# Kernel optimization log

Measured on AMD Instinct MI355X. Metric: run time of the kernel, lower is better.

Reference implementation:

```python
import jax, jax.numpy as jnp
import numpy as np
from jax import lax

B, C, H, W = 16, 256, 80, 80
MID = 64
BN_EPS = 1e-5

SOBEL_X = jnp.array([[-1., 0., 1.], [-2., 0., 2.], [-1., 0., 1.]], jnp.float32) / 8.0
SOBEL_Y = jnp.array([[-1., -2., -1.], [0., 0., 0.], [1., 2., 1.]], jnp.float32) / 8.0
HAAR_LH = jnp.array([[1., -1.], [1., -1.]], jnp.float32) / 2.0
HAAR_HL = jnp.array([[1., 1.], [-1., -1.]], jnp.float32) / 2.0

DN = ('NCHW', 'OIHW', 'NCHW')

def dwconv(x, k2d, pad):
    # depthwise conv: same 2d kernel applied to every channel independently
    c = x.shape[1]
    k = jnp.broadcast_to(k2d[None, None], (c, 1) + k2d.shape)
    return lax.conv_general_dilated(x, k, (1, 1), [(pad, pad), (pad, pad)],
                                    dimension_numbers=DN, feature_group_count=c)

def avg_pool5(x):
    # matches F.avg_pool2d(k=5, s=1, p=2) with count_include_pad=True (divide by 25 always)
    s = lax.reduce_window(x, 0.0, lax.add, (1, 1, 5, 5), (1, 1, 1, 1),
                          [(0, 0), (0, 0), (2, 2), (2, 2)])
    return s / 25.0

def local_variance(x):
    m = avg_pool5(x)
    msq = avg_pool5(x * x)
    return jnp.clip(msq - m * m, 0.0, None)

def bn_silu(x, g, b, m, v):
    # inference batchnorm + SiLU, per-channel params over dim 1
    scale = (g / jnp.sqrt(v + BN_EPS))[None, :, None, None]
    shift = (b - m * g / jnp.sqrt(v + BN_EPS))[None, :, None, None]
    return jax.nn.silu(x * scale + shift)

def setup_inputs() -> dict:
    key = jax.random.key(0)
    ks = jax.random.split(key, 12)
    return {
        'x': jax.random.normal(ks[0], (B, C, H, W), jnp.float32),
        'proj_w': jax.random.normal(ks[1], (MID, C), jnp.float32) * 0.05,
        'bn1_g': jax.random.uniform(ks[2], (MID,), jnp.float32),
        'bn1_b': jax.random.normal(ks[3], (MID,), jnp.float32) * 0.1,
        'bn1_m': jax.random.normal(ks[4], (MID,), jnp.float32) * 0.1,
        'bn1_v': jax.random.uniform(ks[5], (MID,), jnp.float32) + 0.5,
        'fuse1_w': jax.random.normal(ks[6], (MID, MID + 2, 3, 3), jnp.float32) * 0.05,
        'bn2_g': jax.random.uniform(ks[7], (MID,), jnp.float32),
        'bn2_b': jax.random.normal(ks[8], (MID,), jnp.float32) * 0.1,
        'bn2_m': jax.random.normal(ks[9], (MID,), jnp.float32) * 0.1,
        'bn2_v': jax.random.uniform(ks[10], (MID,), jnp.float32) + 0.5,
        'fuse2_w': jax.random.normal(ks[11], (1, MID), jnp.float32) * 0.1,
    }

def reference(x, proj_w, bn1_g, bn1_b, bn1_m, bn1_v,
              fuse1_w, bn2_g, bn2_b, bn2_m, bn2_v, fuse2_w):
    b, c, h, w = x.shape
    # --- edge density ---
    gx = dwconv(x, SOBEL_X, 1)
    gy = dwconv(x, SOBEL_Y, 1)
    edge = jnp.sqrt(gx * gx + gy * gy).mean(axis=1, keepdims=True)  # (B,1,H,W)
    edge_density = edge / (avg_pool5(edge) + 1e-6)
    # --- periodicity ---
    lh = dwconv(x, HAAR_LH, 0)  # (B,C,H-1,W-1)
    hl = dwconv(x, HAAR_HL, 0)
    lh = jax.image.resize(lh, (b, c, h, w), method='bilinear')  # half-pixel, matches align_corners=False
    hl = jax.image.resize(hl, (b, c, h, w), method='bilinear')
    period = jnp.sqrt(local_variance(lh) + local_variance(hl) + 1e-6).mean(axis=1, keepdims=True)
    # --- feat_proj: 1x1 conv + BN + SiLU ---
    feat = bn_silu(jnp.einsum('bchw,mc->bmhw', x, proj_w), bn1_g, bn1_b, bn1_m, bn1_v)
    # --- fuse: 3x3 conv + BN + SiLU -> 1x1 conv -> sigmoid ---
    combined = jnp.concatenate([feat, edge_density, period], axis=1)  # (B,MID+2,H,W)
    y = lax.conv_general_dilated(combined, fuse1_w, (1, 1), [(1, 1), (1, 1)], dimension_numbers=DN)
    y = bn_silu(y, bn2_g, bn2_b, bn2_m, bn2_v)
    weight = jax.nn.sigmoid(jnp.einsum('bmhw,om->bohw', y, fuse2_w))  # (B,1,H,W)
    return x * weight
```

## Files before the change

### kernel.cpp

```cpp
#include <hip/hip_runtime.h>
#include <hip/hip_bf16.h>
#include <math.h>

#define HWN 6400
#define CC 256
#define MIDN 64
#define NCG 64

typedef _Float16 f16x8 __attribute__((ext_vector_type(8)));
typedef _Float16 f16x4 __attribute__((ext_vector_type(4)));
typedef _Float16 h2    __attribute__((ext_vector_type(2)));
typedef float    f32x4 __attribute__((ext_vector_type(4)));
typedef int      i32x4 __attribute__((ext_vector_type(4)));

__device__ __forceinline__ h2 pk2(float a, float b) {
    return __builtin_bit_cast(h2, __builtin_amdgcn_cvt_pkrtz(a, b));
}
__device__ __forceinline__ float h2lo(h2 v) { return (float)v[0]; }
__device__ __forceinline__ float h2hi(h2 v) { return (float)v[1]; }
__device__ __forceinline__ unsigned h2u(h2 v) { return __builtin_bit_cast(unsigned, v); }
__device__ __forceinline__ h2 u2h(unsigned u) { return __builtin_bit_cast(h2, u); }
__device__ __forceinline__ float vsqrtf_(float x) { float r; asm("v_sqrt_f32 %0, %1" : "=v"(r) : "v"(x)); return r; }

__global__ void prep_kernel(const float* __restrict__ proj_w,
                            const float* __restrict__ g1, const float* __restrict__ b1,
                            const float* __restrict__ m1, const float* __restrict__ v1,
                            const float* __restrict__ f1w,
                            const float* __restrict__ g2, const float* __restrict__ b2,
                            const float* __restrict__ m2, const float* __restrict__ v2,
                            _Float16* __restrict__ apack_proj,
                            _Float16* __restrict__ apack_fuse,
                            float* __restrict__ bias1, float* __restrict__ bias2) {
    int gid = blockIdx.x * blockDim.x + threadIdx.x;
    int stride = gridDim.x * blockDim.x;
    if (gid < MIDN) {
        float s1 = g1[gid] * rsqrtf(v1[gid] + 1e-5f);
        bias1[gid] = b1[gid] - m1[gid] * s1;
        float s2 = g2[gid] * rsqrtf(v2[gid] + 1e-5f);
        bias2[gid] = b2[gid] - m2[gid] * s2;
    }
    for (int i = gid; i < 8 * 4 * 64 * 8; i += stride) {
        int j = i & 7, lane = (i >> 3) & 63, w = (i >> 9) & 3, c = i >> 11;
        int m = w * 16 + (lane & 15);
        int ch = c * 32 + (lane >> 4) * 8 + j;
        float s1 = g1[m] * rsqrtf(v1[m] + 1e-5f);
        apack_proj[i] = (_Float16)(proj_w[m * CC + ch] * s1);
    }
    for (int i = gid; i < 9 * 3 * 4 * 64 * 8; i += stride) {
        int j = i & 7, lane = (i >> 3) & 63, w = (i >> 9) & 3;
        int tc = i >> 11; int c = tc % 3, t = tc / 3;
        int m = w * 16 + (lane & 15);
        int ch = c * 32 + (lane >> 4) * 8 + j;
        float s2 = g2[m] * rsqrtf(v2[m] + 1e-5f);
        float v = 0.f;
        if (ch < 66) v = f1w[(m * 66 + ch) * 9 + t] * s2;
        apack_fuse[i] = (_Float16)v;
    }
}

__launch_bounds__(512, 4)
__global__ void edge_period_kernel(const float* __restrict__ x,
                                   unsigned* __restrict__ part) {
    __shared__ unsigned wb[8][88];
    volatile unsigned (*wbv)[88] = wb;
    int tid = threadIdx.x;
    int w = tid >> 6, l = tid & 63;
    int b = blockIdx.y, cg = blockIdx.x;
    int row0 = w * 10;
    int im1 = (l + 63) & 63, ip1 = (l + 1) & 63;
    bool is0 = (l == 0), is63 = (l == 63), isB = (l < 16);

    if (l < 4) wbv[w][(l < 2) ? l : 80 + l] = 0u;

    float cwA = (l <= 0) ? 1.f : ((l >= 79) ? 0.f : (0.99375f - 0.0125f * (float)l));
    int cB = 64 + l;
    float cwB = (cB >= 79) ? 0.f : (0.99375f - 0.0125f * (float)cB);
    h2 v_pk = pk2(0.5f * cwA, 0.5f * cwB);
    h2 u_pk = pk2(0.5f * (1.f - cwA), 0.5f * (1.f - cwB));

    h2 erh[10], prh[10];
#pragma unroll
    for (int k = 0; k < 10; k++) { erh[k] = u2h(0u); prh[k] = u2h(0u); }

#pragma unroll 1
    for (int ch = 0; ch < 4; ch++) {
        const float* xch = x + ((size_t)(b * CC + cg * 4 + ch)) * HWN;
        auto rawload = [&](int rr, float& a, float& bb) {
            a = 0.f; bb = 0.f;
            if (rr >= 0 && rr < 80) {
                a = xch[rr * 80 + l];
                if (isB) bb = xch[rr * 80 + 64 + l];
            }
        };
        auto mktrip = [&](float a, float bb, h2& t0, h2& t1, h2& t2) {
            h2 xc = pk2(a, bb);
            int xi = __builtin_bit_cast(int, xc);
            unsigned um = (unsigned)__shfl(xi, im1);
            unsigned up = (unsigned)__shfl(xi, ip1);
            um = is0 ? ((um & 0xFFFFu) << 16) : um;
            up = is63 ? (up >> 16) : up;
            t0 = u2h(um); t1 = xc; t2 = u2h(up);
        };
        h2 xm1_0, xm1_1, xm1_2, x0_0, x0_1, x0_2, xp1_0, xp1_1, xp1_2;
        float ta, tb, ra, rb, na, nb;
        rawload(row0 - 3, ta, tb);
        rawload(row0 - 2, ra, rb);
        mktrip(ta, tb, xm1_0, xm1_1, xm1_2);
        mktrip(ra, rb, x0_0, x0_1, x0_2);
        rawload(row0 - 1, ra, rb);
        h2 lhc_p, hlc_p;
        {
            h2 sa = xm1_0 + x0_0, sb = xm1_1 + x0_1, sc2 = xm1_2 + x0_2;
            h2 da = xm1_0 - x0_0, db = xm1_1 - x0_1, dc = xm1_2 - x0_2;
            lhc_p = u_pk * (sa - sb) + v_pk * (sb - sc2);
            hlc_p = u_pk * (da + db) + v_pk * (db + dc);
        }
        h2 ringA[5], ringB[5], ringS[5];
#pragma unroll
        for (int s = 0; s < 14; s++) {
            int r = row0 - 2 + s;
            if (s < 13) rawload(row0 + s, na, nb);
            mktrip(ra, rb, xp1_0, xp1_1, xp1_2);
            if (s >= 2 && s < 12) {
                h2 gx = (xm1_2 - xm1_0) + (x0_2 - x0_0) + (x0_2 - x0_0) + (xp1_2 - xp1_0);
                h2 gy = (xp1_0 - xm1_0) + (xp1_1 - xm1_1) + (xp1_1 - xm1_1) + (xp1_2 - xm1_2);
                h2 g2v = gx * gx + gy * gy;
                erh[s - 2] += pk2(vsqrtf_(h2lo(g2v)) * 0.125f, vsqrtf_(h2hi(g2v)) * 0.125f);
            }
            h2 sa = x0_0 + xp1_0, sb = x0_1 + xp1_1, sc2 = x0_2 + xp1_2;
            h2 da = x0_0 - xp1_0, db = x0_1 - xp1_1, dc = x0_2 - xp1_2;
            h2 lhc = u_pk * (sa - sb) + v_pk * (sb - sc2);
            h2 hlc = u_pk * (da + db) + v_pk * (db + dc);
            float cw = (r <= 0) ? 1.f : ((r >= 79) ? 0.f : (0.99375f - 0.0125f * (float)r));
            h2 cwp = pk2(cw, cw), pwp = pk2(1.f - cw, 1.f - cw);
            h2 lhr = pwp * lhc_p + cwp * lhc;
            h2 hlr = pwp * hlc_p + cwp * hlc;
            lhc_p = lhc; hlc_p = hlc;
            unsigned lu = h2u(lhr), hu = h2u(hlr);
            unsigned fA = (lu & 0xFFFFu) | (hu << 16);
            unsigned fB = (lu >> 16) | (hu & 0xFFFF0000u);
            bool fv = (r >= 0) && (r < 80);
            if (!fv) { fA = 0u; fB = 0u; }
            wbv[w][2 + l] = fA;
            if (isB) wbv[w][66 + l] = fB;
            unsigned am2 = wbv[w][l], am1 = wbv[w][l + 1], ap1 = wbv[w][l + 3], ap2 = wbv[w][l + 4];
            unsigned bm2 = 0, bm1 = 0, bp1 = 0, bp2 = 0;
            if (isB) { bm2 = wbv[w][64 + l]; bm1 = wbv[w][65 + l]; bp1 = wbv[w][67 + l]; bp2 = wbv[w][68 + l]; }
            h2 fAh = u2h(fA), fBh = u2h(fB);
            h2 n0 = u2h(am2), n1 = u2h(am1), n2 = u2h(ap1), n3 = u2h(ap2);
            h2 hA = fAh + n0 + n1 + n2 + n3;
            h2 qa = fAh * fAh + n0 * n0 + n1 * n1 + n2 * n2 + n3 * n3;
            float s2A = h2lo(qa) + h2hi(qa);
            h2 m0 = u2h(bm2), m1 = u2h(bm1), m2 = u2h(bp1), m3 = u2h(bp2);
            h2 hB = fBh + m0 + m1 + m2 + m3;
            h2 qb = fBh * fBh + m0 * m0 + m1 * m1 + m2 * m2 + m3 * m3;
            float s2B = h2lo(qb) + h2hi(qb);
            ringA[s % 5] = hA; ringB[s % 5] = hB;
            ringS[s % 5] = pk2(s2A, s2B);
            if (s >= 4) {
                h2 SA = ringA[0] + ringA[1] + ringA[2] + ringA[3] + ringA[4];
                h2 SB = ringB[0] + ringB[1] + ringB[2] + ringB[3] + ringB[4];
                h2 S2 = ringS[0] + ringS[1] + ringS[2] + ringS[3] + ringS[4];
                float SLA = h2lo(SA), SHA = h2hi(SA);
                float SLB = h2lo(SB), SHB = h2hi(SB);
                float vA = 0.04f * h2lo(S2) - 0.0016f * (SLA * SLA + SHA * SHA);
                float vB = 0.04f * h2hi(S2) - 0.0016f * (SLB * SLB + SHB * SHB);
                vA = fmaxf(vA, 0.f) + 1e-6f;
                vB = fmaxf(vB, 0.f) + 1e-6f;
                prh[s - 4] += pk2(vsqrtf_(vA), vsqrtf_(vB));
            }
            xm1_0 = x0_0; xm1_1 = x0_1; xm1_2 = x0_2;
            x0_0 = xp1_0; x0_1 = xp1_1; x0_2 = xp1_2;
            ra = na; rb = nb;
        }
    }
    size_t base = ((size_t)(cg * 16 + b) * 80 + row0) * 80;
#pragma unroll
    for (int k = 0; k < 10; k++) {
        unsigned eu = h2u(erh[k]), pu = h2u(prh[k]);
        part[base + k * 80 + l] = (eu & 0xFFFFu) | (pu << 16);
        if (isB) part[base + k * 80 + 64 + l] = (eu >> 16) | (pu & 0xFFFF0000u);
    }
}

__launch_bounds__(256)
__global__ void density_kernel(const unsigned* __restrict__ part,
                               _Float16* __restrict__ feat_t) {
    __shared__ float E[14][84];
    __shared__ float Hs[14][84];
    __shared__ float Ps[10][80];
    int band = blockIdx.x, b = blockIdx.y, tid = threadIdx.x;
    int r0 = band * 10;
    if (tid < 56) { int rr = tid >> 2, c4 = tid & 3; E[rr][(c4 < 2) ? c4 : 80 + c4] = 0.f; }
    for (int idx = tid; idx < 14 * 80; idx += 256) {
        int rr = idx / 80, j = idx - rr * 80;
        int row = r0 - 2 + rr;
        float e = 0.f, p = 0.f;
        if (row >= 0 && row < 80) {
            size_t off = ((size_t)b * 80 + row) * 80 + j;
#pragma unroll 4
            for (int g = 0; g < NCG; g++) {
                h2 v = u2h(part[(size_t)g * (16 * 80 * 80) + off]);
                e += h2lo(v); p += h2hi(v);
            }
        }
        E[rr][2 + j] = e * (1.f / 256.f);
        if (rr >= 2 && rr < 12) Ps[rr - 2][j] = p * (1.f / 256.f);
    }
    __syncthreads();
    for (int idx = tid; idx < 14 * 80; idx += 256) {
        int rr = idx / 80, j = idx - rr * 80;
        Hs[rr][2 + j] = E[rr][j] + E[rr][j + 1] + E[rr][j + 2] + E[rr][j + 3] + E[rr][j + 4];
    }
    __syncthreads();
    for (int idx = tid; idx < 10 * 80; idx += 256) {
        int k = idx / 80, j = idx - k * 80;
        int rr = k + 2;
        float pool = Hs[rr - 2][2 + j] + Hs[rr - 1][2 + j] + Hs[rr][2 + j]
                   + Hs[rr + 1][2 + j] + Hs[rr + 2][2 + j];
        float ed = E[rr][2 + j] / (pool * 0.04f + 1e-6f);
        _Float16* fp = feat_t + ((size_t)(b * HWN) + (r0 + k) * 80 + j) * 96;
        f16x8 z8 = {};
        f16x8 f8 = {};
        f8[0] = (_Float16)ed; f8[1] = (_Float16)Ps[k][j];
        *reinterpret_cast<f16x8*>(fp + 64) = f8;
        *reinterpret_cast<f16x8*>(fp + 72) = z8;
        *reinterpret_cast<f16x8*>(fp + 80) = z8;
        *reinterpret_cast<f16x8*>(fp + 88) = z8;
    }
}

__launch_bounds__(256)
__global__ void proj_kernel(const float* __restrict__ x,
                            const _Float16* __restrict__ apack,
                            const float* __restrict__ bias1,
                            _Float16* __restrict__ feat_t) {
    __shared__ __align__(16) unsigned char lds[64 * 512];
    int b = blockIdx.y, p0 = blockIdx.x * 64;
    int tid = threadIdx.x, w = tid >> 6, l = tid & 63;

#pragma unroll 4
    for (int i = 0; i < 16; i++) {
        int ch0 = i * 16 + w * 4;
        f16x4 v4;
#pragma unroll
        for (int q = 0; q < 4; q++)
            v4[q] = (_Float16)x[((size_t)(b * CC + ch0 + q)) * HWN + p0 + l];
        int byte = l * 512 + ((ch0 * 2) ^ ((l & 7) << 4));
        *reinterpret_cast<f16x4*>(lds + byte) = v4;
    }
    __syncthreads();

    const f16x8* Ap = reinterpret_cast<const f16x8*>(apack);
    f32x4 acc[4];
#pragma unroll
    for (int ct = 0; ct < 4; ct++) acc[ct] = (f32x4){0.f, 0.f, 0.f, 0.f};

    int kb = 16 * (l >> 4);
#pragma unroll 2
    for (int c = 0; c < 8; c++) {
        f16x8 a = Ap[(c * 4 + w) * 64 + l];
#pragma unroll
        for (int ct = 0; ct < 4; ct++) {
            int byte = (ct * 16 + (l & 15)) * 512 + ((c * 64 + kb) ^ ((l & 7) << 4));
            f16x8 bv = *reinterpret_cast<const f16x8*>(lds + byte);
            acc[ct] = __builtin_amdgcn_mfma_f32_16x16x32_f16(a, bv, acc[ct], 0, 0, 0);
        }
    }

    float b1v[4];
#pragma unroll
    for (int q = 0; q < 4; q++) b1v[q] = bias1[w * 16 + (l >> 4) * 4 + q];
#pragma unroll
    for (int ct = 0; ct < 4; ct++) {
        f16x4 o4;
#pragma unroll
        for (int q = 0; q < 4; q++) {
            float z = acc[ct][q] + b1v[q];
            o4[q] = (_Float16)(z / (1.f + expf(-z)));
        }
        size_t px = (size_t)(b * HWN) + p0 + ct * 16 + (l & 15);
        *reinterpret_cast<f16x4*>(feat_t + px * 96 + w * 16 + (l >> 4) * 4) = o4;
    }
}

#define TROW 256
__launch_bounds__(256)
__global__ void fuse_kernel(const _Float16* __restrict__ feat_t,
                            const _Float16* __restrict__ apack,
                            const float* __restrict__ bias2,
                            const float* __restrict__ fuse2,
                            const float* __restrict__ x,
                            float* __restrict__ out) {
    __shared__ __align__(16) unsigned char tl[108 * TROW];
    __shared__ float R[4 * 4 * 4 * 16];
    __shared__ float wgtbuf[64];
    int b = blockIdx.y, t5 = blockIdx.x;
    int ti = t5 / 5, tj = t5 - ti * 5;
    int i0 = ti * 4, j0 = tj * 16;
    int tid = threadIdx.x, w = tid >> 6, l = tid & 63;

    for (int idx = tid; idx < 1296; idx += 256) {
        int hpx = idx / 12, g = idx - hpx * 12;
        int hr = hpx / 18, hc = hpx - hr * 18;
        int gi = i0 - 1 + hr, gj = j0 - 1 + hc;
        i32x4 val = {0, 0, 0, 0};
        if (gi >= 0 && gi < 80 && gj >= 0 && gj < 80) {
            val = *reinterpret_cast<const i32x4*>(
                feat_t + ((size_t)(b * HWN) + gi * 80 + gj) * 96 + g * 8);
        }
        *reinterpret_cast<i32x4*>(tl + hpx * TROW + ((g * 16) ^ ((hc & 7) << 4))) = val;
    }
    __syncthreads();

    const f16x8* Ap = reinterpret_cast<const f16x8*>(apack);
    f32x4 acc[4];
#pragma unroll
    for (int r = 0; r < 4; r++) acc[r] = (f32x4){0.f, 0.f, 0.f, 0.f};
    int kb = 16 * (l >> 4);

#pragma unroll 1
    for (int t = 0; t < 9; t++) {
        int dy = t / 3, dx = t - dy * 3;
        f16x8 a0 = Ap[((t * 3 + 0) * 4 + w) * 64 + l];
        f16x8 a1 = Ap[((t * 3 + 1) * 4 + w) * 64 + l];
        f16x8 a2 = Ap[((t * 3 + 2) * 4 + w) * 64 + l];
        int hc = (l & 15) + dx;
        int key = (hc & 7) << 4;
#pragma unroll
        for (int r = 0; r < 4; r++) {
            int base = ((r + dy) * 18 + hc) * TROW;
            f16x8 b0 = *reinterpret_cast<const f16x8*>(tl + base + ((0 + kb) ^ key));
            acc[r] = __builtin_amdgcn_mfma_f32_16x16x32_f16(a0, b0, acc[r], 0, 0, 0);
            f16x8 b1_ = *reinterpret_cast<const f16x8*>(tl + base + ((64 + kb) ^ key));
            acc[r] = __builtin_amdgcn_mfma_f32_16x16x32_f16(a1, b1_, acc[r], 0, 0, 0);
            f16x8 b2_ = *reinterpret_cast<const f16x8*>(tl + base + ((128 + kb) ^ key));
            acc[r] = __builtin_amdgcn_mfma_f32_16x16x32_f16(a2, b2_, acc[r], 0, 0, 0);
        }
    }

    float b2v[4], f2v[4];
#pragma unroll
    for (int q = 0; q < 4; q++) {
        int m = w * 16 + (l >> 4) * 4 + q;
        b2v[q] = bias2[m];
        f2v[q] = fuse2[m];
    }
#pragma unroll
    for (int r = 0; r < 4; r++) {
        float p = 0.f;
#pragma unroll
        for (int q = 0; q < 4; q++) {
            float z = acc[r][q] + b2v[q];
            p += f2v[q] * (z / (1.f + expf(-z)));
        }
        R[((w * 4 + r) * 4 + (l >> 4)) * 16 + (l & 15)] = p;
    }
    __syncthreads();
    if (tid < 64) {
        int r = tid >> 4, cc = tid & 15;
        float s = 0.f;
#pragma unroll
        for (int w2 = 0; w2 < 4; w2++)
#pragma unroll
            for (int g2 = 0; g2 < 4; g2++)
                s += R[((w2 * 4 + r) * 4 + g2) * 16 + cc];
        wgtbuf[tid] = 1.f / (1.f + expf(-s));
    }
    __syncthreads();

    int r = l >> 4, cc = l & 15;
    float wgt = wgtbuf[l];
    size_t base = (size_t)b * CC * HWN + (size_t)((i0 + r) * 80 + j0 + cc);
    const float* xp = x + base;
    float* op = out + base;
#pragma unroll 4
    for (int ch = w * 64; ch < w * 64 + 64; ch++) {
        op[(size_t)ch * HWN] = xp[(size_t)ch * HWN] * wgt;
    }
}

extern "C" void kernel_launch(void* const* d_in, const int* in_sizes, int n_in,
                              void* d_out, int out_size, void* d_ws, size_t ws_size,
                              hipStream_t stream) {
    (void)in_sizes; (void)n_in; (void)out_size; (void)ws_size;
    const float* x       = (const float*)d_in[0];
    const float* proj_w  = (const float*)d_in[1];
    const float* bn1_g   = (const float*)d_in[2];
    const float* bn1_b   = (const float*)d_in[3];
    const float* bn1_m   = (const float*)d_in[4];
    const float* bn1_v   = (const float*)d_in[5];
    const float* fuse1_w = (const float*)d_in[6];
    const float* bn2_g   = (const float*)d_in[7];
    const float* bn2_b   = (const float*)d_in[8];
    const float* bn2_m   = (const float*)d_in[9];
    const float* bn2_v   = (const float*)d_in[10];
    const float* fuse2_w = (const float*)d_in[11];
    float* out = (float*)d_out;

    float* ws = (float*)d_ws;
    unsigned* part        = (unsigned*)ws;
    _Float16* feat_t      = (_Float16*)(ws + 6553600);
    _Float16* apack_proj  = (_Float16*)(ws + 11468800);
    _Float16* apack_fuse  = (_Float16*)(ws + 11476992);
    float*    bias1       = ws + 11504640;
    float*    bias2       = ws + 11504704;

    prep_kernel<<<288, 256, 0, stream>>>(proj_w, bn1_g, bn1_b, bn1_m, bn1_v,
                                         fuse1_w, bn2_g, bn2_b, bn2_m, bn2_v,
                                         apack_proj, apack_fuse, bias1, bias2);
    edge_period_kernel<<<dim3(NCG, 16), 512, 0, stream>>>(x, part);
    density_kernel<<<dim3(8, 16), 256, 0, stream>>>(part, feat_t);
    proj_kernel<<<dim3(100, 16), 256, 0, stream>>>(x, apack_proj, bias1, feat_t);
    fuse_kernel<<<dim3(100, 16), 256, 0, stream>>>(feat_t, apack_fuse,
                                                   bias2, fuse2_w, x, out);
}
```

Measured before the change: 265.1 us.

## Add per-channel edge/period kernel and separate channel-sum reduction stage

Adds a new edge/period kernel that gives each block a single channel instead of accumulating a group of 4 channels. This raises the block count and shortens per-thread loops, at the cost of writing a partial buffer 4x larger (256 groups) to the workspace. The channel reduction moves out of the density kernel into a new fully parallel chsum kernel, so density no longer loops over the groups. The per-channel path is chosen only when the workspace is large enough; otherwise it falls back to the old accumulating kernel.

```diff
diff --git a/kernel.cpp b/kernel.cpp
--- a/kernel.cpp
+++ b/kernel.cpp
@@ -5,7 +5,6 @@
 #define HWN 6400
 #define CC 256
 #define MIDN 64
-#define NCG 64
 
 typedef _Float16 f16x8 __attribute__((ext_vector_type(8)));
 typedef _Float16 f16x4 __attribute__((ext_vector_type(4)));
@@ -58,9 +57,132 @@
     }
 }
 
+__launch_bounds__(256, 4)
+__global__ void edge_period_pc_kernel(const float* __restrict__ x,
+                                      unsigned* __restrict__ part) {
+    __shared__ unsigned wb[4][88];
+    volatile unsigned (*wbv)[88] = wb;
+    int tid = threadIdx.x;
+    int w = tid >> 6, l = tid & 63;
+    int b = blockIdx.y, cg = blockIdx.x;
+    int row0 = w * 20;
+    int im1 = (l + 63) & 63, ip1 = (l + 1) & 63;
+    bool is0 = (l == 0), is63 = (l == 63), isB = (l < 16);
+
+    if (l < 4) wbv[w][(l < 2) ? l : 80 + l] = 0u;
+
+    float cwA = (l <= 0) ? 1.f : ((l >= 79) ? 0.f : (0.99375f - 0.0125f * (float)l));
+    int cB = 64 + l;
+    float cwB = (cB >= 79) ? 0.f : (0.99375f - 0.0125f * (float)cB);
+    h2 v_pk = pk2(0.5f * cwA, 0.5f * cwB);
+    h2 u_pk = pk2(0.5f * (1.f - cwA), 0.5f * (1.f - cwB));
+
+    h2 ering[2];
+    ering[0] = u2h(0u); ering[1] = u2h(0u);
+
+    const float* xch = x + ((size_t)(b * CC + cg)) * HWN;
+    unsigned* pout = part + ((size_t)(cg * 16 + b)) * HWN;
+
+    auto rawload = [&](int rr, float& a, float& bb) {
+        a = 0.f; bb = 0.f;
+        if (rr >= 0 && rr < 80) {
+            a = xch[rr * 80 + l];
+            if (isB) bb = xch[rr * 80 + 64 + l];
+        }
+    };
+    auto mktrip = [&](float a, float bb, h2& t0, h2& t1, h2& t2) {
+        h2 xc = pk2(a, bb);
+        int xi = __builtin_bit_cast(int, xc);
+        unsigned um = (unsigned)__shfl(xi, im1);
+        unsigned up = (unsigned)__shfl(xi, ip1);
+        um = is0 ? ((um & 0xFFFFu) << 16) : um;
+        up = is63 ? (up >> 16) : up;
+        t0 = u2h(um); t1 = xc; t2 = u2h(up);
+    };
+    h2 xm1_0, xm1_1, xm1_2, x0_0, x0_1, x0_2, xp1_0, xp1_1, xp1_2;
+    float ta, tb, ra, rb, na, nb;
+    rawload(row0 - 3, ta, tb);
+    rawload(row0 - 2, ra, rb);
+    mktrip(ta, tb, xm1_0, xm1_1, xm1_2);
+    mktrip(ra, rb, x0_0, x0_1, x0_2);
+    rawload(row0 - 1, ra, rb);
+    h2 lhc_p, hlc_p;
+    {
+        h2 sa = xm1_0 + x0_0, sb = xm1_1 + x0_1, sc2 = xm1_2 + x0_2;
+        h2 da = xm1_0 - x0_0, db = xm1_1 - x0_1, dc = xm1_2 - x0_2;
+        lhc_p = u_pk * (sa - sb) + v_pk * (sb - sc2);
+        hlc_p = u_pk * (da + db) + v_pk * (db + dc);
+    }
+    h2 ringA[5], ringB[5], ringS[5];
+#pragma unroll
+    for (int s = 0; s < 24; s++) {
+        int r = row0 - 2 + s;
+        if (s < 23) rawload(row0 + s, na, nb);
+        mktrip(ra, rb, xp1_0, xp1_1, xp1_2);
+        h2 er_new = u2h(0u);
+        if (s >= 2 && s < 22) {
+            h2 gx = (xm1_2 - xm1_0) + (x0_2 - x0_0) + (x0_2 - x0_0) + (xp1_2 - xp1_0);
+            h2 gy = (xp1_0 - xm1_0) + (xp1_1 - xm1_1) + (xp1_1 - xm1_1) + (xp1_2 - xm1_2);
+            h2 g2v = gx * gx + gy * gy;
+            er_new = pk2(vsqrtf_(h2lo(g2v)) * 0.125f, vsqrtf_(h2hi(g2v)) * 0.125f);
+        }
+        h2 sa = x0_0 + xp1_0, sb = x0_1 + xp1_1, sc2 = x0_2 + xp1_2;
+        h2 da = x0_0 - xp1_0, db = x0_1 - xp1_1, dc = x0_2 - xp1_2;
+        h2 lhc = u_pk * (sa - sb) + v_pk * (sb - sc2);
+        h2 hlc = u_pk * (da + db) + v_pk * (db + dc);
+        float cw = (r <= 0) ? 1.f : ((r >= 79) ? 0.f : (0.99375f - 0.0125f * (float)r));
+        h2 cwp = pk2(cw, cw), pwp = pk2(1.f - cw, 1.f - cw);
+        h2 lhr = pwp * lhc_p + cwp * lhc;
+        h2 hlr = pwp * hlc_p + cwp * hlc;
+        lhc_p = lhc; hlc_p = hlc;
+        unsigned lu = h2u(lhr), hu = h2u(hlr);
+        unsigned fA = (lu & 0xFFFFu) | (hu << 16);
+        unsigned fB = (lu >> 16) | (hu & 0xFFFF0000u);
+        bool fv = (r >= 0) && (r < 80);
+        if (!fv) { fA = 0u; fB = 0u; }
+        wbv[w][2 + l] = fA;
+        if (isB) wbv[w][66 + l] = fB;
+        unsigned am2 = wbv[w][l], am1 = wbv[w][l + 1], ap1 = wbv[w][l + 3], ap2 = wbv[w][l + 4];
+        unsigned bm2 = 0, bm1 = 0, bp1 = 0, bp2 = 0;
+        if (isB) { bm2 = wbv[w][64 + l]; bm1 = wbv[w][65 + l]; bp1 = wbv[w][67 + l]; bp2 = wbv[w][68 + l]; }
+        h2 fAh = u2h(fA), fBh = u2h(fB);
+        h2 n0 = u2h(am2), n1 = u2h(am1), n2 = u2h(ap1), n3 = u2h(ap2);
+        h2 hA = fAh + n0 + n1 + n2 + n3;
+        h2 qa = fAh * fAh + n0 * n0 + n1 * n1 + n2 * n2 + n3 * n3;
+        float s2A = h2lo(qa) + h2hi(qa);
+        h2 m0 = u2h(bm2), m1 = u2h(bm1), m2 = u2h(bp1), m3 = u2h(bp2);
+        h2 hB = fBh + m0 + m1 + m2 + m3;
+        h2 qb = fBh * fBh + m0 * m0 + m1 * m1 + m2 * m2 + m3 * m3;
+        float s2B = h2lo(qb) + h2hi(qb);
+        ringA[s % 5] = hA; ringB[s % 5] = hB;
+        ringS[s % 5] = pk2(s2A, s2B);
+        if (s >= 4) {
+            h2 SA = ringA[0] + ringA[1] + ringA[2] + ringA[3] + ringA[4];
+            h2 SB = ringB[0] + ringB[1] + ringB[2] + ringB[3] + ringB[4];
+            h2 S2 = ringS[0] + ringS[1] + ringS[2] + ringS[3] + ringS[4];
+            float SLA = h2lo(SA), SHA = h2hi(SA);
+            float SLB = h2lo(SB), SHB = h2hi(SB);
+            float vA = 0.04f * h2lo(S2) - 0.0016f * (SLA * SLA + SHA * SHA);
+            float vB = 0.04f * h2hi(S2) - 0.0016f * (SLB * SLB + SHB * SHB);
+            vA = fmaxf(vA, 0.f) + 1e-6f;
+            vB = fmaxf(vB, 0.f) + 1e-6f;
+            unsigned eu = h2u(ering[s & 1]);
+            unsigned pu = h2u(pk2(vsqrtf_(vA), vsqrtf_(vB)));
+            int orow = row0 + s - 4;
+            pout[orow * 80 + l] = (eu & 0xFFFFu) | (pu << 16);
+            if (isB) pout[orow * 80 + 64 + l] = (eu >> 16) | (pu & 0xFFFF0000u);
+        }
+        if (s >= 2 && s < 22) ering[s & 1] = er_new;
+        xm1_0 = x0_0; xm1_1 = x0_1; xm1_2 = x0_2;
+        x0_0 = xp1_0; x0_1 = xp1_1; x0_2 = xp1_2;
+        ra = na; rb = nb;
+    }
+}
+
+#define NCGB 64
 __launch_bounds__(512, 4)
-__global__ void edge_period_kernel(const float* __restrict__ x,
-                                   unsigned* __restrict__ part) {
+__global__ void edge_period_acc_kernel(const float* __restrict__ x,
+                                       unsigned* __restrict__ part) {
     __shared__ unsigned wb[8][88];
     volatile unsigned (*wbv)[88] = wb;
     int tid = threadIdx.x;
@@ -184,7 +306,24 @@
 }
 
 __launch_bounds__(256)
-__global__ void density_kernel(const unsigned* __restrict__ part,
+__global__ void chsum_kernel(const unsigned* __restrict__ part,
+                             float* __restrict__ esum, float* __restrict__ psum,
+                             int ngroups) {
+    int b = blockIdx.y;
+    int p = blockIdx.x * 256 + threadIdx.x;
+    float e = 0.f, pp = 0.f;
+#pragma unroll 8
+    for (int g = 0; g < ngroups; g++) {
+        h2 v = u2h(part[((size_t)(g * 16 + b)) * HWN + p]);
+        e += h2lo(v); pp += h2hi(v);
+    }
+    esum[b * HWN + p] = e;
+    psum[b * HWN + p] = pp;
+}
+
+__launch_bounds__(256)
+__global__ void density_kernel(const float* __restrict__ esum,
+                               const float* __restrict__ psum,
                                _Float16* __restrict__ feat_t) {
     __shared__ float E[14][84];
     __shared__ float Hs[14][84];
@@ -197,12 +336,8 @@
         int row = r0 - 2 + rr;
         float e = 0.f, p = 0.f;
         if (row >= 0 && row < 80) {
-            size_t off = ((size_t)b * 80 + row) * 80 + j;
-#pragma unroll 4
-            for (int g = 0; g < NCG; g++) {
-                h2 v = u2h(part[(size_t)g * (16 * 80 * 80) + off]);
-                e += h2lo(v); p += h2hi(v);
-            }
+            size_t off = (size_t)b * HWN + row * 80 + j;
+            e = esum[off]; p = psum[off];
         }
         E[rr][2 + j] = e * (1.f / 256.f);
         if (rr >= 2 && rr < 12) Ps[rr - 2][j] = p * (1.f / 256.f);
@@ -383,7 +518,7 @@
 extern "C" void kernel_launch(void* const* d_in, const int* in_sizes, int n_in,
                               void* d_out, int out_size, void* d_ws, size_t ws_size,
                               hipStream_t stream) {
-    (void)in_sizes; (void)n_in; (void)out_size; (void)ws_size;
+    (void)in_sizes; (void)n_in; (void)out_size;
     const float* x       = (const float*)d_in[0];
     const float* proj_w  = (const float*)d_in[1];
     const float* bn1_g   = (const float*)d_in[2];
@@ -398,19 +533,35 @@
     const float* fuse2_w = (const float*)d_in[11];
     float* out = (float*)d_out;
 
+    const size_t needA = (size_t)(256 * 16 * HWN) * 4
+                       + (size_t)2 * 16 * HWN * 4
+                       + (size_t)16 * HWN * 96 * 2
+                       + (16384 + 55296) * 2 + 1024;
+    bool useA = ws_size >= needA;
+    int ngroups = useA ? 256 : NCGB;
+
     float* ws = (float*)d_ws;
+    size_t partN = (size_t)ngroups * 16 * HWN;
     unsigned* part        = (unsigned*)ws;
-    _Float16* feat_t      = (_Float16*)(ws + 6553600);
-    _Float16* apack_proj  = (_Float16*)(ws + 11468800);
-    _Float16* apack_fuse  = (_Float16*)(ws + 11476992);
-    float*    bias1       = ws + 11504640;
-    float*    bias2       = ws + 11504704;
+    float*    esum        = ws + partN;
+    float*    psum        = esum + 16 * HWN;
+    _Float16* feat_t      = (_Float16*)(psum + 16 * HWN);
+    float*    after_feat  = (float*)(feat_t + (size_t)16 * HWN * 96);
+    _Float16* apack_proj  = (_Float16*)after_feat;
+    _Float16* apack_fuse  = apack_proj + 16384;
+    float*    bias1       = (float*)(apack_fuse + 55296);
+    float*    bias2       = bias1 + 64;
 
     prep_kernel<<<288, 256, 0, stream>>>(proj_w, bn1_g, bn1_b, bn1_m, bn1_v,
                                          fuse1_w, bn2_g, bn2_b, bn2_m, bn2_v,
                                          apack_proj, apack_fuse, bias1, bias2);
-    edge_period_kernel<<<dim3(NCG, 16), 512, 0, stream>>>(x, part);
-    density_kernel<<<dim3(8, 16), 256, 0, stream>>>(part, feat_t);
+    if (useA) {
+        edge_period_pc_kernel<<<dim3(256, 16), 256, 0, stream>>>(x, part);
+    } else {
+        edge_period_acc_kernel<<<dim3(NCGB, 16), 512, 0, stream>>>(x, part);
+    }
+    chsum_kernel<<<dim3(25, 16), 256, 0, stream>>>(part, esum, psum, ngroups);
+    density_kernel<<<dim3(8, 16), 256, 0, stream>>>(esum, psum, feat_t);
     proj_kernel<<<dim3(100, 16), 256, 0, stream>>>(x, apack_proj, bias1, feat_t);
     fuse_kernel<<<dim3(100, 16), 256, 0, stream>>>(feat_t, apack_fuse,
                                                    bias2, fuse2_w, x, out);
```

After: 218.1 us. 1.22x faster.
